# Optimization experiments

Hardware: AMD Instinct MI355X
Metric: run time of the kernel (lower is better)

Reference implementation:

```python
import jax, jax.numpy as jnp
import numpy as np

B, C, H, W = 16, 128, 32, 32
D, K = 64, 8192
BN_EPS = 1e-5
KLD_SCALE = 10.0
COMMIT = 0.25


def setup_inputs() -> dict:
    key = jax.random.key(0)
    ks = jax.random.split(key, 4)
    return {
        "z": jax.random.normal(ks[0], (B, C, H, W), dtype=jnp.float32),
        "proj_w": jax.random.normal(ks[1], (D, C), dtype=jnp.float32) * (1.0 / np.sqrt(C)),
        "proj_b": jax.random.normal(ks[2], (D,), dtype=jnp.float32) * 0.01,
        "gamma": jnp.ones((D,), dtype=jnp.float32),
        "beta": jnp.zeros((D,), dtype=jnp.float32),
        "running_mean": jnp.zeros((D,), dtype=jnp.float32),
        "running_var": jnp.ones((D,), dtype=jnp.float32),
        "embed": jax.random.normal(ks[3], (K, D), dtype=jnp.float32) * 0.1,
    }


def reference(z, proj_w, proj_b, gamma, beta, running_mean, running_var, embed):
    sg = jax.lax.stop_gradient
    b, c, h, w = z.shape
    # 1x1 conv projection: [B,C,H,W] -> [B,D,H,W]
    x = jnp.einsum('bchw,dc->bdhw', z, proj_w) + proj_b[None, :, None, None]
    # BatchNorm2d (inference mode: running stats)
    scale = gamma * jax.lax.rsqrt(running_var + BN_EPS)
    x = x * scale[None, :, None, None] + (beta - running_mean * scale)[None, :, None, None]
    # NCHW -> NHWC, flatten to [N, D]
    z_e = jnp.transpose(x, (0, 2, 3, 1))
    flat = z_e.reshape(-1, z_e.shape[-1])  # [N, D]
    # pairwise squared distances [N, K]
    dist = (jnp.sum(flat * flat, axis=1, keepdims=True)
            - 2.0 * flat @ embed.T
            + jnp.sum(embed * embed, axis=1)[None, :])
    ind = jnp.argmax(-dist, axis=1).reshape(b, h, w)  # [B,H,W]
    z_q = embed[ind]  # [B,H,W,D] codebook gather
    diff = KLD_SCALE * (COMMIT * jnp.mean((sg(z_q) - z_e) ** 2)
                        + jnp.mean((z_q - sg(z_e)) ** 2))
    z_q_st = z_e + sg(z_q - z_e)  # straight-through
    return jnp.transpose(z_q_st, (0, 3, 1, 2)), diff, ind
```

## Files before the change

### kernel.cpp

```cpp
#include <hip/hip_runtime.h>
#include <math.h>

#define B_   16
#define C_   128
#define H_   32
#define W_   32
#define D_   64
#define K_   8192
#define HW_  (H_*W_)
#define N_   (B_*HW_)

#define CS      16
#define CPB     (K_/CS)
#define CHUNK   128
#define NCH     (CPB/CHUNK)
#define ROWS_PB 256
#define MARGIN  0.12f
#define CAND_CAP 32

typedef short v8s __attribute__((ext_vector_type(8)));
typedef float v4f __attribute__((ext_vector_type(4)));

__device__ __forceinline__ short f2bf(float f) {
    union { float fv; unsigned u; } cv; cv.fv = f;
    unsigned u = cv.u;
    unsigned rnd = ((u >> 16) & 1u) + 0x7fffu;
    return (short)((u + rnd) >> 16);
}

#define GLOAD_LDS16(gp, lp) __builtin_amdgcn_global_load_lds( \
    (const __attribute__((address_space(1))) unsigned int*)(gp), \
    (__attribute__((address_space(3))) unsigned int*)(lp), 16, 0, 0)

__device__ __forceinline__ float exact_score(const float4* __restrict__ zr,
                                             const float* __restrict__ embed,
                                             float h, int k)
{
    const float4* ep = (const float4*)(embed + (size_t)k * D_);
    float sa = 0.f, sb = 0.f;
    #pragma unroll
    for (int d4 = 0; d4 < 16; d4 += 2) {
        float4 ea = ep[d4], eb = ep[d4 + 1];
        sa += ea.x*zr[d4].x + ea.y*zr[d4].y + ea.z*zr[d4].z + ea.w*zr[d4].w;
        sb += eb.x*zr[d4+1].x + eb.y*zr[d4+1].y + eb.z*zr[d4+1].z + eb.w*zr[d4+1].w;
    }
    return (sa + sb) - h;
}

__global__ __launch_bounds__(256) void k_proj(
    const float* __restrict__ z, const float* __restrict__ pw,
    const float* __restrict__ pb, const float* __restrict__ gamma,
    const float* __restrict__ beta, const float* __restrict__ rmean,
    const float* __restrict__ rvar, float* __restrict__ ze,
    short* __restrict__ zbf)
{
    __shared__ float zt[64][132];
    __shared__ float wl[64][132];
    const int tid = threadIdx.x;
    const int n0  = blockIdx.x * 64;
    const int b   = n0 / HW_;
    const int hw0 = n0 % HW_;
    const float* zb = z + (size_t)b * C_ * HW_ + hw0;

    #pragma unroll
    for (int it = 0; it < 32; ++it) {
        int flat = tid + 256 * it;
        int c = flat >> 6, p = flat & 63;
        zt[p][c] = zb[c * HW_ + p];
    }
    #pragma unroll
    for (int it = 0; it < 32; ++it) {
        int flat = tid + 256 * it;
        int d = flat >> 7, c = flat & 127;
        wl[d][c] = pw[d * C_ + c];
    }
    __syncthreads();

    const int tp = tid & 15;
    const int td = tid >> 4;
    float acc[4][4] = {};
    #pragma unroll
    for (int c4 = 0; c4 < 32; ++c4) {
        float4 zv[4], wv[4];
        #pragma unroll
        for (int i = 0; i < 4; ++i) zv[i] = *(const float4*)&zt[4*tp + i][4*c4];
        #pragma unroll
        for (int j = 0; j < 4; ++j) wv[j] = *(const float4*)&wl[4*td + j][4*c4];
        #pragma unroll
        for (int i = 0; i < 4; ++i)
            #pragma unroll
            for (int j = 0; j < 4; ++j)
                acc[i][j] += zv[i].x*wv[j].x + zv[i].y*wv[j].y
                           + zv[i].z*wv[j].z + zv[i].w*wv[j].w;
    }

    float sc[4], bi[4];
    #pragma unroll
    for (int j = 0; j < 4; ++j) {
        int d = 4*td + j;
        float s = gamma[d] / sqrtf(rvar[d] + 1e-5f);
        sc[j] = s;
        bi[j] = pb[d] * s + beta[d] - rmean[d] * s;
    }
    #pragma unroll
    for (int i = 0; i < 4; ++i) {
        int n = n0 + 4*tp + i;
        float4 o;
        o.x = acc[i][0]*sc[0] + bi[0];
        o.y = acc[i][1]*sc[1] + bi[1];
        o.z = acc[i][2]*sc[2] + bi[2];
        o.w = acc[i][3]*sc[3] + bi[3];
        *(float4*)&ze[(size_t)n * D_ + 4*td] = o;
        short4 ob;
        ob.x = f2bf(o.x); ob.y = f2bf(o.y); ob.z = f2bf(o.z); ob.w = f2bf(o.w);
        *(short4*)&zbf[(size_t)n * D_ + 4*td] = ob;
    }
}

__global__ __launch_bounds__(256) void k_prep(const float* __restrict__ e,
                                              float* __restrict__ hn,
                                              short* __restrict__ ebs)
{
    int t = blockIdx.x * 256 + threadIdx.x;
    float4 v = ((const float4*)e)[t];
    float s = v.x*v.x + v.y*v.y + v.z*v.z + v.w*v.w;
    s += __shfl_xor(s, 1);
    s += __shfl_xor(s, 2);
    s += __shfl_xor(s, 4);
    s += __shfl_xor(s, 8);
    if ((threadIdx.x & 15) == 0) hn[t >> 4] = 0.5f * s;

    const int k = t >> 4, p = t & 15;
    if (p < 8) {
        const int j = p ^ (k & 7);
        const float* src = e + (size_t)k * D_ + j * 8;
        v8s o;
        #pragma unroll
        for (int i = 0; i < 8; ++i) o[i] = f2bf(src[i]);
        *(v8s*)(ebs + (size_t)k * D_ + p * 8) = o;
    }
}

template<bool PUSH>
__global__ __launch_bounds__(256) void k_sweep(
    const short* __restrict__ zbf, const short* __restrict__ ebs,
    const float* __restrict__ hn, float* __restrict__ pbest,
    const float* __restrict__ Vm, int* __restrict__ cnt,
    int* __restrict__ cand)
{
    __shared__ short eb[2][CHUNK * 64];
    __shared__ float hl[2][CHUNK];
    const int tid  = threadIdx.x;
    const int lane = tid & 63;
    const int wv   = tid >> 6;
    const int q    = lane >> 4;
    const int l15  = lane & 15;
    const int m8   = l15 & 7;
    const int rowBase = blockIdx.x * ROWS_PB + wv * 64;
    const int code0   = blockIdx.y * CPB;

    v8s A[4][2];
    #pragma unroll
    for (int rt = 0; rt < 4; ++rt)
        #pragma unroll
        for (int f = 0; f < 2; ++f)
            A[rt][f] = *(const v8s*)(zbf + (size_t)(rowBase + rt*16 + l15) * D_
                                      + f*32 + q*8);

    float best[4][4];
    float vm[4][4];
    if (PUSH) {
        #pragma unroll
        for (int rt = 0; rt < 4; ++rt)
            #pragma unroll
            for (int r = 0; r < 4; ++r)
                vm[rt][r] = Vm[rowBase + rt*16 + q*4 + r];
    } else {
        #pragma unroll
        for (int rt = 0; rt < 4; ++rt)
            #pragma unroll
            for (int r = 0; r < 4; ++r) best[rt][r] = -INFINITY;
    }

    const int rb0 = l15 * 64 + ((q ^ m8) * 8);
    const int rb1 = l15 * 64 + (((q ^ m8) ^ 4) * 8);

    const char* srcBase = (const char*)(ebs + (size_t)code0 * 64);
    #define STAGE(b, ch) do {                                              \
        const char* s_ = srcBase + (size_t)(ch) * (CHUNK * 128);           \
        char* l_ = (char*)&eb[(b)][0];                                     \
        _Pragma("unroll")                                                  \
        for (int i_ = 0; i_ < 4; ++i_) {                                   \
            int seg_ = (wv * 4 + i_) * 1024 + lane * 16;                   \
            GLOAD_LDS16(s_ + seg_, l_ + seg_);                             \
        }                                                                  \
        if (tid < CHUNK) hl[(b)][tid] = hn[code0 + (ch) * CHUNK + tid];    \
    } while (0)

    STAGE(0, 0);
    __syncthreads();

    #pragma unroll 1
    for (int ch = 0; ch < NCH; ++ch) {
        const int buf = ch & 1;
        if (ch + 1 < NCH) STAGE(buf ^ 1, ch + 1);
        const int c0 = code0 + ch * CHUNK;
        const short* ep = &eb[buf][0];

        #pragma unroll
        for (int t = 0; t < CHUNK / 16; ++t) {
            v8s B0 = *(const v8s*)(ep + rb0 + t * 1024);
            v8s B1 = *(const v8s*)(ep + rb1 + t * 1024);
            const float mh = -hl[buf][t * 16 + l15];
            #pragma unroll
            for (int rt = 0; rt < 4; ++rt) {
                v4f c = {mh, mh, mh, mh};
                c = __builtin_amdgcn_mfma_f32_16x16x32_bf16(A[rt][0], B0, c, 0, 0, 0);
                c = __builtin_amdgcn_mfma_f32_16x16x32_bf16(A[rt][1], B1, c, 0, 0, 0);
                if (!PUSH) {
                    #pragma unroll
                    for (int r = 0; r < 4; ++r) best[rt][r] = fmaxf(best[rt][r], c[r]);
                } else {
                    bool a0 = c[0] > vm[rt][0];
                    bool a1 = c[1] > vm[rt][1];
                    bool a2 = c[2] > vm[rt][2];
                    bool a3 = c[3] > vm[rt][3];
                    if (a0 | a1 | a2 | a3) {
                        const int code = c0 + t * 16 + l15;
                        const int row0 = rowBase + rt*16 + q*4;
                        #pragma unroll
                        for (int r = 0; r < 4; ++r) {
                            if (c[r] > vm[rt][r]) {
                                int s = atomicAdd(&cnt[row0 + r], 1);
                                if (s < CAND_CAP) cand[(row0 + r) * CAND_CAP + s] = code;
                            }
                        }
                    }
                }
            }
        }
        __syncthreads();
    }
    #undef STAGE

    if (!PUSH) {
        #pragma unroll
        for (int rt = 0; rt < 4; ++rt)
            #pragma unroll
            for (int r = 0; r < 4; ++r) {
                float v = best[rt][r];
                v = fmaxf(v, __shfl_xor(v, 1));
                v = fmaxf(v, __shfl_xor(v, 2));
                v = fmaxf(v, __shfl_xor(v, 4));
                v = fmaxf(v, __shfl_xor(v, 8));
                if (l15 == 0)
                    pbest[(size_t)blockIdx.y * N_ + rowBase + rt*16 + q*4 + r] = v;
            }
    }
}

__global__ __launch_bounds__(256) void k_comb(const float* __restrict__ pbest,
                                              float* __restrict__ Vm,
                                              int* __restrict__ cnt)
{
    int n = blockIdx.x * 256 + threadIdx.x;
    float v = -INFINITY;
    #pragma unroll
    for (int s = 0; s < CS; ++s) v = fmaxf(v, pbest[(size_t)s * N_ + n]);
    Vm[n] = v - MARGIN;
    cnt[n] = 0;
}

__global__ __launch_bounds__(64) void k_pick(
    const int* __restrict__ cnt, const int* __restrict__ cand,
    const float* __restrict__ embed, const float* __restrict__ hn,
    const float* __restrict__ ze, float* __restrict__ out0,
    float* __restrict__ outIdx, float* __restrict__ bsum)
{
    const int tid = threadIdx.x;
    const int n   = blockIdx.x * 64 + tid;

    float4 zr[16];
    const float4* zp = (const float4*)(ze + (size_t)n * D_);
    #pragma unroll
    for (int i = 0; i < 16; ++i) zr[i] = zp[i];

    const int m = cnt[n];
    float best = -INFINITY;
    int   bidx = 0x7fffffff;
    if (m > CAND_CAP) {
        for (int k = 0; k < K_; ++k) {
            float s = exact_score(zr, embed, hn[k], k);
            if (s > best) { best = s; bidx = k; }
        }
    } else {
        for (int i = 0; i < m; ++i) {
            int k = cand[n * CAND_CAP + i];
            float s = exact_score(zr, embed, hn[k], k);
            if (s > best || (s == best && k < bidx)) { best = s; bidx = k; }
        }
    }
    if (bidx == 0x7fffffff) bidx = 0;
    outIdx[n] = (float)bidx;

    const float4* eq = (const float4*)(embed + (size_t)bidx * D_);
    const int b = n >> 10, hw = n & 1023;
    float* o = out0 + (size_t)b * (D_ * HW_) + hw;

    float local = 0.f;
    #pragma unroll
    for (int d4 = 0; d4 < 16; ++d4) {
        float4 e = eq[d4], zv = zr[d4];
        float dx = e.x - zv.x, dy = e.y - zv.y, dz = e.z - zv.z, dw = e.w - zv.w;
        local += dx*dx + dy*dy + dz*dz + dw*dw;
        o[(4*d4 + 0) * HW_] = e.x;
        o[(4*d4 + 1) * HW_] = e.y;
        o[(4*d4 + 2) * HW_] = e.z;
        o[(4*d4 + 3) * HW_] = e.w;
    }

    local += __shfl_xor(local, 1);
    local += __shfl_xor(local, 2);
    local += __shfl_xor(local, 4);
    local += __shfl_xor(local, 8);
    local += __shfl_xor(local, 16);
    local += __shfl_xor(local, 32);
    if (tid == 0) bsum[blockIdx.x] = local;
}

__global__ __launch_bounds__(256) void k_diff(const float* __restrict__ bsum,
                                              float* __restrict__ outd)
{
    __shared__ float red[256];
    float s = bsum[threadIdx.x];
    red[threadIdx.x] = s;
    __syncthreads();
    for (int st = 128; st > 0; st >>= 1) {
        if (threadIdx.x < st) red[threadIdx.x] += red[threadIdx.x + st];
        __syncthreads();
    }
    if (threadIdx.x == 0) *outd = red[0] * (12.5f / (float)(N_ * D_));
}

extern "C" void kernel_launch(void* const* d_in, const int* in_sizes, int n_in,
                              void* d_out, int out_size, void* d_ws, size_t ws_size,
                              hipStream_t stream)
{
    const float* z     = (const float*)d_in[0];
    const float* pw    = (const float*)d_in[1];
    const float* pb    = (const float*)d_in[2];
    const float* gamma = (const float*)d_in[3];
    const float* beta  = (const float*)d_in[4];
    const float* rmean = (const float*)d_in[5];
    const float* rvar  = (const float*)d_in[6];
    const float* embed = (const float*)d_in[7];

    float* out = (float*)d_out;
    float* out0    = out;
    float* outDiff = out + (size_t)N_ * D_;
    float* outIdx  = outDiff + 1;

    float* ws    = (float*)d_ws;
    float* ze    = ws;
    short* zbf   = (short*)(ze + (size_t)N_ * D_);
    short* ebs   = zbf + (size_t)N_ * D_;
    float* hn    = (float*)(ebs + (size_t)K_ * D_);
    float* pbest = hn + K_;
    float* Vm    = pbest + (size_t)CS * N_;
    int*   cnt   = (int*)(Vm + N_);
    int*   cand  = cnt + N_;
    float* bsum  = (float*)(cand + (size_t)N_ * CAND_CAP);

    k_proj <<<N_ / 64, 256, 0, stream>>>(z, pw, pb, gamma, beta, rmean, rvar, ze, zbf);
    k_prep <<<(K_ * 16) / 256, 256, 0, stream>>>(embed, hn, ebs);
    k_sweep<false><<<dim3(N_ / ROWS_PB, CS), 256, 0, stream>>>(
        zbf, ebs, hn, pbest, nullptr, nullptr, nullptr);
    k_comb <<<N_ / 256, 256, 0, stream>>>(pbest, Vm, cnt);
    k_sweep<true><<<dim3(N_ / ROWS_PB, CS), 256, 0, stream>>>(
        zbf, ebs, hn, pbest, Vm, cnt, cand);
    k_pick <<<N_ / 64, 64, 0, stream>>>(cnt, cand, embed, hn, ze, out0, outIdx, bsum);
    k_diff <<<1, 256, 0, stream>>>(bsum, outDiff);
}
```

Baseline: 170.4 us.

## Fuse projection with codebook prep, drop diff kernel, halve sweep chunk size

The codebook bf16/norm prep is merged into the projection kernel as extra blocks, which removes one launch. The final diff reduction kernel is replaced by per-block atomicAdd into the output, zeroed in k_comb. The sweep chunk size drops from 128 to 64 codes, which shrinks LDS use and may raise occupancy. Rows with zero candidates now fall back to a full scan. Atomic accumulation makes the diff sum order nondeterministic.

```diff
diff --git a/kernel.cpp b/kernel.cpp
--- a/kernel.cpp
+++ b/kernel.cpp
@@ -12,7 +12,7 @@
 
 #define CS      16
 #define CPB     (K_/CS)
-#define CHUNK   128
+#define CHUNK   64
 #define NCH     (CPB/CHUNK)
 #define ROWS_PB 256
 #define MARGIN  0.12f
@@ -47,16 +47,39 @@
     return (sa + sb) - h;
 }
 
-__global__ __launch_bounds__(256) void k_proj(
+__global__ __launch_bounds__(256) void k_projprep(
     const float* __restrict__ z, const float* __restrict__ pw,
     const float* __restrict__ pb, const float* __restrict__ gamma,
     const float* __restrict__ beta, const float* __restrict__ rmean,
-    const float* __restrict__ rvar, float* __restrict__ ze,
-    short* __restrict__ zbf)
+    const float* __restrict__ rvar, const float* __restrict__ embed,
+    float* __restrict__ ze, short* __restrict__ zbf,
+    short* __restrict__ ebs, float* __restrict__ hn)
 {
     __shared__ float zt[64][132];
     __shared__ float wl[64][132];
     const int tid = threadIdx.x;
+
+    if (blockIdx.x >= 256) {
+        int t = (blockIdx.x - 256) * 256 + tid;
+        float4 v = ((const float4*)embed)[t];
+        float s = v.x*v.x + v.y*v.y + v.z*v.z + v.w*v.w;
+        s += __shfl_xor(s, 1);
+        s += __shfl_xor(s, 2);
+        s += __shfl_xor(s, 4);
+        s += __shfl_xor(s, 8);
+        const int k = t >> 4, p = t & 15;
+        if (p == 0) hn[k] = 0.5f * s;
+        if (p < 8) {
+            const int j = p ^ (k & 7);
+            const float* src = embed + (size_t)k * D_ + j * 8;
+            v8s o;
+            #pragma unroll
+            for (int i = 0; i < 8; ++i) o[i] = f2bf(src[i]);
+            *(v8s*)(ebs + (size_t)k * D_ + p * 8) = o;
+        }
+        return;
+    }
+
     const int n0  = blockIdx.x * 64;
     const int b   = n0 / HW_;
     const int hw0 = n0 % HW_;
@@ -117,30 +140,6 @@
     }
 }
 
-__global__ __launch_bounds__(256) void k_prep(const float* __restrict__ e,
-                                              float* __restrict__ hn,
-                                              short* __restrict__ ebs)
-{
-    int t = blockIdx.x * 256 + threadIdx.x;
-    float4 v = ((const float4*)e)[t];
-    float s = v.x*v.x + v.y*v.y + v.z*v.z + v.w*v.w;
-    s += __shfl_xor(s, 1);
-    s += __shfl_xor(s, 2);
-    s += __shfl_xor(s, 4);
-    s += __shfl_xor(s, 8);
-    if ((threadIdx.x & 15) == 0) hn[t >> 4] = 0.5f * s;
-
-    const int k = t >> 4, p = t & 15;
-    if (p < 8) {
-        const int j = p ^ (k & 7);
-        const float* src = e + (size_t)k * D_ + j * 8;
-        v8s o;
-        #pragma unroll
-        for (int i = 0; i < 8; ++i) o[i] = f2bf(src[i]);
-        *(v8s*)(ebs + (size_t)k * D_ + p * 8) = o;
-    }
-}
-
 template<bool PUSH>
 __global__ __launch_bounds__(256) void k_sweep(
     const short* __restrict__ zbf, const short* __restrict__ ebs,
@@ -190,8 +189,8 @@
         const char* s_ = srcBase + (size_t)(ch) * (CHUNK * 128);           \
         char* l_ = (char*)&eb[(b)][0];                                     \
         _Pragma("unroll")                                                  \
-        for (int i_ = 0; i_ < 4; ++i_) {                                   \
-            int seg_ = (wv * 4 + i_) * 1024 + lane * 16;                   \
+        for (int i_ = 0; i_ < 2; ++i_) {                                   \
+            int seg_ = (wv * 2 + i_) * 1024 + lane * 16;                   \
             GLOAD_LDS16(s_ + seg_, l_ + seg_);                             \
         }                                                                  \
         if (tid < CHUNK) hl[(b)][tid] = hn[code0 + (ch) * CHUNK + tid];    \
@@ -261,7 +260,8 @@
 
 __global__ __launch_bounds__(256) void k_comb(const float* __restrict__ pbest,
                                               float* __restrict__ Vm,
-                                              int* __restrict__ cnt)
+                                              int* __restrict__ cnt,
+                                              float* __restrict__ outDiff)
 {
     int n = blockIdx.x * 256 + threadIdx.x;
     float v = -INFINITY;
@@ -269,13 +269,14 @@
     for (int s = 0; s < CS; ++s) v = fmaxf(v, pbest[(size_t)s * N_ + n]);
     Vm[n] = v - MARGIN;
     cnt[n] = 0;
+    if (n == 0) *outDiff = 0.f;
 }
 
 __global__ __launch_bounds__(64) void k_pick(
     const int* __restrict__ cnt, const int* __restrict__ cand,
     const float* __restrict__ embed, const float* __restrict__ hn,
     const float* __restrict__ ze, float* __restrict__ out0,
-    float* __restrict__ outIdx, float* __restrict__ bsum)
+    float* __restrict__ outIdx, float* __restrict__ outDiff)
 {
     const int tid = threadIdx.x;
     const int n   = blockIdx.x * 64 + tid;
@@ -288,7 +289,7 @@
     const int m = cnt[n];
     float best = -INFINITY;
     int   bidx = 0x7fffffff;
-    if (m > CAND_CAP) {
+    if (m == 0 || m > CAND_CAP) {
         for (int k = 0; k < K_; ++k) {
             float s = exact_score(zr, embed, hn[k], k);
             if (s > best) { best = s; bidx = k; }
@@ -325,21 +326,7 @@
     local += __shfl_xor(local, 8);
     local += __shfl_xor(local, 16);
     local += __shfl_xor(local, 32);
-    if (tid == 0) bsum[blockIdx.x] = local;
-}
-
-__global__ __launch_bounds__(256) void k_diff(const float* __restrict__ bsum,
-                                              float* __restrict__ outd)
-{
-    __shared__ float red[256];
-    float s = bsum[threadIdx.x];
-    red[threadIdx.x] = s;
-    __syncthreads();
-    for (int st = 128; st > 0; st >>= 1) {
-        if (threadIdx.x < st) red[threadIdx.x] += red[threadIdx.x + st];
-        __syncthreads();
-    }
-    if (threadIdx.x == 0) *outd = red[0] * (12.5f / (float)(N_ * D_));
+    if (tid == 0) atomicAdd(outDiff, local * (12.5f / (float)(N_ * D_)));
 }
 
 extern "C" void kernel_launch(void* const* d_in, const int* in_sizes, int n_in,
@@ -369,15 +356,14 @@
     float* Vm    = pbest + (size_t)CS * N_;
     int*   cnt   = (int*)(Vm + N_);
     int*   cand  = cnt + N_;
-    float* bsum  = (float*)(cand + (size_t)N_ * CAND_CAP);
-
-    k_proj <<<N_ / 64, 256, 0, stream>>>(z, pw, pb, gamma, beta, rmean, rvar, ze, zbf);
-    k_prep <<<(K_ * 16) / 256, 256, 0, stream>>>(embed, hn, ebs);
+
+    k_projprep<<<256 + 512, 256, 0, stream>>>(z, pw, pb, gamma, beta, rmean,
+                                              rvar, embed, ze, zbf, ebs, hn);
     k_sweep<false><<<dim3(N_ / ROWS_PB, CS), 256, 0, stream>>>(
         zbf, ebs, hn, pbest, nullptr, nullptr, nullptr);
-    k_comb <<<N_ / 256, 256, 0, stream>>>(pbest, Vm, cnt);
+    k_comb <<<N_ / 256, 256, 0, stream>>>(pbest, Vm, cnt, outDiff);
     k_sweep<true><<<dim3(N_ / ROWS_PB, CS), 256, 0, stream>>>(
         zbf, ebs, hn, pbest, Vm, cnt, cand);
-    k_pick <<<N_ / 64, 64, 0, stream>>>(cnt, cand, embed, hn, ze, out0, outIdx, bsum);
-    k_diff <<<1, 256, 0, stream>>>(bsum, outDiff);
-}
+    k_pick <<<N_ / 64, 64, 0, stream>>>(cnt, cand, embed, hn, ze, out0,
+                                        outIdx, outDiff);
+}
```

Measured after the change: 172.4 us. About the same (+1.1%).
